# Optimization experiments

Measured on AMD Instinct MI355X. Metric: run time of the kernel, lower is better.

Reference implementation:

```python
import jax, jax.numpy as jnp
import numpy as np

L = 248      # max_clip_seq_len
WIN = 3      # window_size
H = 8        # attention heads
D = 768      # input/output dim
HID = 256    # rope hidden dim
SIGMA = 2.0
EPS_LN = 1e-5


def _layernorm(x, g, b):
    m = jnp.mean(x, axis=-1, keepdims=True)
    v = jnp.var(x, axis=-1, keepdims=True)
    return (x - m) / jnp.sqrt(v + EPS_LN) * g + b


def _normalize(x):
    n = jnp.linalg.norm(x, axis=-1, keepdims=True)
    return x / jnp.maximum(n, 1e-12)


def _peb_forward(word_feat, text_feat_full, word_pos, ctx_W, ctx_b, in_W, in_b,
                 out_W, out_b, cn_g, cn_b, r1_W, r1_b, ln_g, ln_b, r2_W, r2_b,
                 pos_emb, pos_temp):
    B, N, _ = word_feat.shape
    valid = word_pos != -1                              # [B,N] bool
    vf = valid.astype(word_feat.dtype)[..., None]       # [B,N,1]
    wp = jnp.clip(word_pos, 0, L - 1)                   # [B,N]
    half = WIN // 2
    offs = jnp.arange(-half, half + 1)
    positions = jnp.clip(wp[..., None] + offs[None, None, :], 0, L - 1)
    ctx = text_feat_full[jnp.arange(B)[:, None, None], positions]
    ctx_anchor = (ctx.reshape(B, N, WIN * D) @ ctx_W + ctx_b) * vf       # [B,N,D]
    q = word_feat * vf                                  # word_proj is Identity (768->768)
    # MultiheadAttention (batch_first), query=q, key=value=ctx_anchor
    hd = D // H
    qp = (q @ in_W[:, :D] + in_b[:D]).reshape(B, N, H, hd)
    kp = (ctx_anchor @ in_W[:, D:2 * D] + in_b[D:2 * D]).reshape(B, N, H, hd)
    vp = (ctx_anchor @ in_W[:, 2 * D:] + in_b[2 * D:]).reshape(B, N, H, hd)
    scores = jnp.einsum('bqhd,bkhd->bhqk', qp, kp) / jnp.sqrt(jnp.asarray(hd, q.dtype))
    attn = jax.nn.softmax(scores, axis=-1)
    ao = jnp.einsum('bhqk,bkhd->bqhd', attn, vp).reshape(B, N, D)
    attn_out = ao @ out_W + out_b
    x = _layernorm(q + attn_out, cn_g, cn_b) * vf       # word_feat_with_ctx
    # rope_mapping: Linear -> GELU -> LayerNorm -> Linear
    rope = _layernorm(jax.nn.gelu(x @ r1_W + r1_b, approximate=False), ln_g, ln_b) @ r2_W + r2_b
    rope_n = _normalize(rope)
    clip_ref_n = _normalize(pos_emb)                    # [L,D]
    temp = jnp.maximum(pos_temp, 0.001)
    logits = jnp.einsum('bnd,ld->bnl', rope_n, clip_ref_n) / temp
    log_q = jax.nn.log_softmax(logits, axis=-1)
    # gaussian soft target over L positions
    pos_idx = jnp.arange(L, dtype=jnp.float32)
    d2 = (pos_idx[None, None, :] - wp[..., None].astype(jnp.float32)) ** 2
    targ = jnp.exp(-d2 / (2.0 * SIGMA ** 2))
    targ = targ / (targ.sum(axis=-1, keepdims=True) + 1e-12)
    lqv = log_q * vf
    tv = targ * vf
    n_valid = valid.sum().astype(jnp.float32)
    safe_t = jnp.where(tv > 0, tv, 1.0)
    kl = jnp.sum(jnp.where(tv > 0, tv * (jnp.log(safe_t) - lqv), 0.0)) / (n_valid + 1e-12)
    # relative position loss on cosine similarity
    pos_sim01 = (jnp.einsum('bnd,bmd->bnm', rope_n, rope_n) + 1.0) / 2.0
    wpf = wp.astype(jnp.float32)
    target_sim = 1.0 - jnp.abs(wpf[:, :, None] - wpf[:, None, :]) / float(L)
    vm2 = vf[:, :, 0][:, None, :] * vf[:, :, 0][:, :, None]
    rel = jnp.sum((pos_sim01 * vm2 - target_sim * vm2) ** 2) / (vm2.sum() + 1e-12)
    peb_loss = (1.0 * kl + 0.5 * rel) * 1.0             # kl_weight=1, rel_weight=0.5, peb_weight=1
    # scatter blended positional features to 248-length sequence (vectorized over batch)
    vals = 0.8 * pos_emb[wp] + 0.2 * rope               # [B,N,D]
    pos_s = jnp.where(valid, wp, L)                     # invalid -> OOB index, dropped
    emb = jnp.zeros((B, L, D), word_feat.dtype).at[jnp.arange(B)[:, None], pos_s].set(vals, mode='drop')
    return emb, peb_loss, kl, rel


def setup_inputs() -> dict:
    key = jax.random.key(0)
    ks = jax.random.split(key, 20)
    B, N = 128, 128
    word_feat = jax.random.normal(ks[0], (B, N, D), jnp.float32)
    text_feat_full = jax.random.normal(ks[1], (B, L, D), jnp.float32)
    # unique sorted positions per batch (scatter is then deterministic, matching torch)
    perms = jax.vmap(lambda k: jax.random.permutation(k, L))(jax.random.split(ks[2], B))
    word_pos = jnp.sort(perms[:, :N], axis=-1).astype(jnp.int32)
    s = 0.02
    return {
        'word_feat': word_feat,
        'text_feat_full': text_feat_full,
        'word_pos': word_pos,
        'ctx_W': s * jax.random.normal(ks[3], (WIN * D, D), jnp.float32),
        'ctx_b': s * jax.random.normal(ks[4], (D,), jnp.float32),
        'in_W': s * jax.random.normal(ks[5], (D, 3 * D), jnp.float32),
        'in_b': s * jax.random.normal(ks[6], (3 * D,), jnp.float32),
        'out_W': s * jax.random.normal(ks[7], (D, D), jnp.float32),
        'out_b': s * jax.random.normal(ks[8], (D,), jnp.float32),
        'cn_g': jnp.ones((D,), jnp.float32) + s * jax.random.normal(ks[9], (D,), jnp.float32),
        'cn_b': s * jax.random.normal(ks[10], (D,), jnp.float32),
        'r1_W': s * jax.random.normal(ks[11], (D, HID), jnp.float32),
        'r1_b': s * jax.random.normal(ks[12], (HID,), jnp.float32),
        'ln_g': jnp.ones((HID,), jnp.float32) + s * jax.random.normal(ks[13], (HID,), jnp.float32),
        'ln_b': s * jax.random.normal(ks[14], (HID,), jnp.float32),
        'r2_W': s * jax.random.normal(ks[15], (HID, D), jnp.float32),
        'r2_b': s * jax.random.normal(ks[16], (D,), jnp.float32),
        'pos_emb': jax.random.normal(ks[17], (L, D), jnp.float32),
        'pos_temp': jnp.asarray(1.0, jnp.float32),
    }


def reference(word_feat, text_feat_full, word_pos, ctx_W, ctx_b, in_W, in_b,
              out_W, out_b, cn_g, cn_b, r1_W, r1_b, ln_g, ln_b, r2_W, r2_b,
              pos_emb, pos_temp):
    return _peb_forward(word_feat, text_feat_full, word_pos, ctx_W, ctx_b, in_W, in_b,
                        out_W, out_b, cn_g, cn_b, r1_W, r1_b, ln_g, ln_b, r2_W, r2_b,
                        pos_emb, pos_temp)
```

## Files before the change

### kernel.cpp

```cpp
#include <hip/hip_runtime.h>
#include <math.h>

#define BB   128
#define NN   128
#define LL   248
#define DD   768
#define HH   8
#define HDh  96
#define HIDN 256
#define MROWS (BB*NN)
#define MB_   (1u<<20)
#define KVLD 1536

typedef unsigned short u16;
typedef unsigned int   u32;
typedef __attribute__((ext_vector_type(8))) short s16x8;
typedef __attribute__((ext_vector_type(4))) float f32x4;

__device__ __forceinline__ u16 f2bf(float x) {
    u32 u = __float_as_uint(x);
    u32 r = u + 0x7fffu + ((u >> 16) & 1u);
    return (u16)(r >> 16);
}
__device__ __forceinline__ float bf2f(u16 h) {
    return __uint_as_float(((u32)h) << 16);
}
__device__ __forceinline__ void gload16(const void* g, void* l) {
    __builtin_amdgcn_global_load_lds(
        (const __attribute__((address_space(1))) void*)g,
        (__attribute__((address_space(3))) void*)l, 16, 0, 0);
}

template<int NT>
__device__ __forceinline__ float breduce_sum(float v, float* red) {
    const int tid = threadIdx.x;
    red[tid] = v; __syncthreads();
#pragma unroll
    for (int o = NT / 2; o > 0; o >>= 1) {
        if (tid < o) red[tid] += red[tid + o];
        __syncthreads();
    }
    float r = red[0]; __syncthreads();
    return r;
}
__device__ __forceinline__ double breduce_sum_d256(double v, double* red) {
    const int tid = threadIdx.x;
    red[tid] = v; __syncthreads();
#pragma unroll
    for (int o = 128; o > 0; o >>= 1) {
        if (tid < o) red[tid] += red[tid + o];
        __syncthreads();
    }
    double r = red[0]; __syncthreads();
    return r;
}

#define TEXT_N8 (BB*LL*DD/8)
#define Q_N8    (MROWS*(DD/8))
__global__ __launch_bounds__(256)
void prep_all_kernel(const float* __restrict__ ctx_W, u16* __restrict__ ctx_Wt,
                     const float* __restrict__ in_W,  u16* __restrict__ in_Wt,
                     const float* __restrict__ out_W, u16* __restrict__ out_Wt,
                     const float* __restrict__ r1_W,  u16* __restrict__ r1_Wt,
                     const float* __restrict__ r2_W,  u16* __restrict__ r2_Wt,
                     const float* __restrict__ text,  u16* __restrict__ textb,
                     const float* __restrict__ wf,    u16* __restrict__ qb,
                     const int* __restrict__ wpos,    int* __restrict__ cpos,
                     const float* __restrict__ pe,    u16* __restrict__ clipb) {
    __shared__ float smem[32 * 33];
    int bid = blockIdx.x;
    const int tid = threadIdx.x;

    if (bid < 4416) {
        const float* src; u16* dst; int C;
        if (bid < 1728)      { src = ctx_W; dst = ctx_Wt; C = 768;  }
        else if (bid < 3456) { src = in_W;  dst = in_Wt;  C = 2304; bid -= 1728; }
        else if (bid < 4032) { src = out_W; dst = out_Wt; C = 768;  bid -= 3456; }
        else if (bid < 4224) { src = r1_W;  dst = r1_Wt;  C = 256;  bid -= 4032; }
        else                 { src = r2_W;  dst = r2_Wt;  C = 768;  bid -= 4224; }
        const int R = (C == 768) ? ((dst == ctx_Wt) ? 2304 : ((dst == out_Wt) ? 768 : 256))
                                 : ((C == 2304) ? 768 : 768);
        const int ct = C >> 5;
        const int r0 = (bid / ct) * 32, c0 = (bid % ct) * 32;
        const int tx = tid & 31, ty = tid >> 5;
#pragma unroll
        for (int i = 0; i < 32; i += 8)
            smem[(ty + i) * 33 + tx] = src[(size_t)(r0 + ty + i) * C + c0 + tx];
        __syncthreads();
#pragma unroll
        for (int i = 0; i < 32; i += 8)
            dst[(size_t)(c0 + ty + i) * R + r0 + tx] = f2bf(smem[tx * 33 + ty + i]);
    } else if (bid < 4672) {
        const int l = bid - 4416;
        if (l >= LL) {
            for (int j = 0; j < 3; ++j) clipb[(size_t)l * DD + tid + j * 256] = 0;
            return;
        }
        float t[3]; float q = 0.f;
#pragma unroll
        for (int j = 0; j < 3; ++j) {
            t[j] = pe[(size_t)l * DD + tid + j * 256];
            q = fmaf(t[j], t[j], q);
        }
        q = breduce_sum<256>(q, smem);
        float inv = 1.f / fmaxf(sqrtf(q), 1e-12f);
#pragma unroll
        for (int j = 0; j < 3; ++j)
            clipb[(size_t)l * DD + tid + j * 256] = f2bf(t[j] * inv);
    } else {
        const int ebid = bid - 4672;
        if (ebid == 0) {
            for (int r = tid; r < MROWS; r += 256) {
                int w = wpos[r];
                cpos[r] = w < 0 ? 0 : (w > LL - 1 ? LL - 1 : w);
            }
        }
        const int TOT8 = TEXT_N8 + Q_N8;
        const int lane = tid & 63;
        const int wid = ebid * 4 + (tid >> 6);
        const int step = 2048 * 4 * 256;
        for (int base = wid * 256; base < TOT8; base += step) {
            if (base < TEXT_N8) {
                const float4* sp = (const float4*)text;
                float4 v[8]; int g[4];
#pragma unroll
                for (int j = 0; j < 4; ++j) {
                    g[j] = base + j * 64 + lane;
                    v[2*j]   = sp[2 * (size_t)g[j]];
                    v[2*j+1] = sp[2 * (size_t)g[j] + 1];
                }
#pragma unroll
                for (int j = 0; j < 4; ++j) {
                    uint4 o;
                    o.x = (u32)f2bf(v[2*j].x)   | ((u32)f2bf(v[2*j].y)   << 16);
                    o.y = (u32)f2bf(v[2*j].z)   | ((u32)f2bf(v[2*j].w)   << 16);
                    o.z = (u32)f2bf(v[2*j+1].x) | ((u32)f2bf(v[2*j+1].y) << 16);
                    o.w = (u32)f2bf(v[2*j+1].z) | ((u32)f2bf(v[2*j+1].w) << 16);
                    ((uint4*)textb)[g[j]] = o;
                }
            } else {
                const float4* sp = (const float4*)wf;
                float4 v[8]; int g[4]; float vfm[4];
#pragma unroll
                for (int j = 0; j < 4; ++j) {
                    g[j] = base + j * 64 + lane - TEXT_N8;
                    v[2*j]   = sp[2 * (size_t)g[j]];
                    v[2*j+1] = sp[2 * (size_t)g[j] + 1];
                }
#pragma unroll
                for (int j = 0; j < 4; ++j)
                    vfm[j] = (wpos[g[j] / 96] != -1) ? 1.f : 0.f;
#pragma unroll
                for (int j = 0; j < 4; ++j) {
                    uint4 o;
                    o.x = (u32)f2bf(v[2*j].x * vfm[j])   | ((u32)f2bf(v[2*j].y * vfm[j])   << 16);
                    o.y = (u32)f2bf(v[2*j].z * vfm[j])   | ((u32)f2bf(v[2*j].w * vfm[j])   << 16);
                    o.z = (u32)f2bf(v[2*j+1].x * vfm[j]) | ((u32)f2bf(v[2*j+1].y * vfm[j]) << 16);
                    o.w = (u32)f2bf(v[2*j+1].z * vfm[j]) | ((u32)f2bf(v[2*j+1].w * vfm[j]) << 16);
                    ((uint4*)qb)[g[j]] = o;
                }
            }
        }
    }
}

template<int GATHER, int CBF16, int MASK>
__global__ __launch_bounds__(256)
void gemm_bt(const u16* __restrict__ A,
             const u16* __restrict__ TXT,
             const int* __restrict__ cpos,
             const u16* __restrict__ Bt,
             const float* __restrict__ bias,
             void* __restrict__ Cout, int ldc, int K,
             const int* __restrict__ wpos) {
    __shared__ __align__(16) u16 Alds[128 * 64];
    __shared__ __align__(16) u16 Blds[128 * 64];
    const int tid = threadIdx.x;
    const int l = tid & 63, wv = tid >> 6;

    const int gx  = gridDim.x;
    const int hw  = blockIdx.y * gx + blockIdx.x;
    const int nwg = gx * gridDim.y;
    const int cpx = nwg >> 3;
    const int lin = (hw & 7) * cpx + (hw >> 3);
    const int m0 = (lin / gx) * 128, n0 = (lin % gx) * 128;

    const int rw = wv * 8 + (l >> 3);
    const int ce = ((l & 7) ^ (l >> 3)) << 3;
    u16* Ad0 = Alds + wv * 512;
    u16* Bd0 = Blds + wv * 512;

    const int wm = (wv >> 1) * 64, wn = (wv & 1) * 64;
    const int la = l & 15, lg = l >> 4;

    int aoff[4], boff[4];
#pragma unroll
    for (int m = 0; m < 4; ++m) {
        int ra = wm + m * 16 + la;
        aoff[m] = ra * 64 + (((lg ^ (la & 7)) << 3));
        int rb = wn + m * 16 + la;
        boff[m] = rb * 64 + (((lg ^ (la & 7)) << 3));
    }

    const u16* pb[4];
#pragma unroll
    for (int i = 0; i < 4; ++i)
        pb[i] = Bt + (size_t)(n0 + rw + i * 32) * K + ce;

    f32x4 acc[4][4] = {};

    auto do_step = [&](const u16* a0, const u16* a1, const u16* a2, const u16* a3,
                       const u16* b0, const u16* b1, const u16* b2, const u16* b3) {
        gload16(a0, Ad0);
        gload16(a1, Ad0 + 2048);
        gload16(a2, Ad0 + 4096);
        gload16(a3, Ad0 + 6144);
        gload16(b0, Bd0);
        gload16(b1, Bd0 + 2048);
        gload16(b2, Bd0 + 4096);
        gload16(b3, Bd0 + 6144);
        __syncthreads();
#pragma unroll
        for (int kk = 0; kk < 2; ++kk) {
            const int kx = kk << 5;
            s16x8 af[4], bf[4];
#pragma unroll
            for (int m = 0; m < 4; ++m) af[m] = *(const s16x8*)(Alds + (aoff[m] ^ kx));
#pragma unroll
            for (int n = 0; n < 4; ++n) bf[n] = *(const s16x8*)(Blds + (boff[n] ^ kx));
#pragma unroll
            for (int m = 0; m < 4; ++m)
#pragma unroll
                for (int n = 0; n < 4; ++n)
                    acc[m][n] = __builtin_amdgcn_mfma_f32_16x16x32_bf16(
                        af[m], bf[n], acc[m][n], 0, 0, 0);
        }
        __syncthreads();
    };

    if constexpr (GATHER) {
        int gb[4], gc[4];
#pragma unroll
        for (int i = 0; i < 4; ++i) {
            int g = m0 + rw + i * 32;
            gb[i] = g >> 7;
            gc[i] = cpos[g];
        }
#pragma unroll 1
        for (int w = 0; w < 3; ++w) {
            const u16* pa[4];
#pragma unroll
            for (int i = 0; i < 4; ++i) {
                int p = gc[i] + w - 1;
                p = p < 0 ? 0 : (p > LL - 1 ? LL - 1 : p);
                pa[i] = TXT + ((size_t)(gb[i] * LL + p)) * DD + ce;
            }
            const u16* b0 = pb[0] + w * DD; const u16* b1 = pb[1] + w * DD;
            const u16* b2 = pb[2] + w * DD; const u16* b3 = pb[3] + w * DD;
#pragma unroll 1
            for (int kt = 0; kt < 12; ++kt)
                do_step(pa[0] + kt * 64, pa[1] + kt * 64, pa[2] + kt * 64, pa[3] + kt * 64,
                        b0 + kt * 64, b1 + kt * 64, b2 + kt * 64, b3 + kt * 64);
        }
    } else {
        const u16* pa[4];
#pragma unroll
        for (int i = 0; i < 4; ++i)
            pa[i] = A + (size_t)(m0 + rw + i * 32) * K + ce;
        const int nk = K >> 6;
#pragma unroll 1
        for (int kt = 0; kt < nk; ++kt)
            do_step(pa[0] + kt * 64, pa[1] + kt * 64, pa[2] + kt * 64, pa[3] + kt * 64,
                    pb[0] + kt * 64, pb[1] + kt * 64, pb[2] + kt * 64, pb[3] + kt * 64);
    }

#pragma unroll
    for (int m = 0; m < 4; ++m) {
        const int rb = m0 + wm + m * 16 + lg * 4;
        float vf[4];
        if constexpr (MASK) {
#pragma unroll
            for (int r = 0; r < 4; ++r) vf[r] = (wpos[rb + r] != -1) ? 1.f : 0.f;
        }
#pragma unroll
        for (int n = 0; n < 4; ++n) {
            const int col = n0 + wn + n * 16 + la;
            const float bv = bias[col];
#pragma unroll
            for (int r = 0; r < 4; ++r) {
                float o = acc[m][n][r] + bv;
                if constexpr (MASK) o *= vf[r];
                if constexpr (CBF16)
                    ((u16*)Cout)[(size_t)(rb + r) * ldc + col] = f2bf(o);
                else
                    ((float*)Cout)[(size_t)(rb + r) * ldc + col] = o;
            }
        }
    }
}

__global__ __launch_bounds__(512)
void attn_mfma_kernel(const u16* __restrict__ qp, const u16* __restrict__ kvb,
                      u16* __restrict__ ao) {
    __shared__ __align__(16) u16 K_lds[128 * 96];
    __shared__ __align__(16) u16 Vt_lds[96 * 128];
    __shared__ __align__(16) u16 P_lds[128 * 128];
    const int bh = blockIdx.x;
    const int b = bh >> 3, h = bh & 7;
    const int tid = threadIdx.x;
    const int l = tid & 63, wv = tid >> 6;
    const int la = l & 15, lg = l >> 4;
    const float scale = 0.10206207261596575f;

    const size_t qbase  = ((size_t)b * NN) * DD + h * HDh;
    const size_t kvbase = ((size_t)b * NN) * KVLD + h * HDh;

#pragma unroll
    for (int i = 0; i < 3; ++i) {
        int f = i * 8192 + wv * 1024 + l * 16;
        int row = f / 192;
        int inner = f - row * 192;
        gload16((const char*)(kvb + kvbase + (size_t)row * KVLD) + inner,
                (char*)K_lds + f);
    }

    uint4 vchunk[3]; int vkey[3], vd0[3];
#pragma unroll
    for (int i = 0; i < 3; ++i) {
        int c = tid + i * 512;
        int key = c / 12, dc = c - key * 12;
        vkey[i] = key; vd0[i] = dc * 8;
        vchunk[i] = *(const uint4*)(kvb + kvbase + (size_t)key * KVLD + DD + dc * 8);
    }

    const int q0 = wv * 16;
    s16x8 qf[3];
#pragma unroll
    for (int kt = 0; kt < 3; ++kt)
        qf[kt] = *(const s16x8*)(qp + qbase + (size_t)(q0 + la) * DD + kt * 32 + lg * 8);

#pragma unroll
    for (int i = 0; i < 3; ++i) {
        const u16* e = (const u16*)&vchunk[i];
#pragma unroll
        for (int j = 0; j < 8; ++j) {
            int d = vd0[i] + j;
            int byte = ((d * 128 + vkey[i]) * 2) ^ ((d & 7) << 4);
            *(u16*)((char*)Vt_lds + byte) = e[j];
        }
    }
    __syncthreads();

    f32x4 sacc[8] = {};
#pragma unroll
    for (int kt = 0; kt < 3; ++kt) {
#pragma unroll
        for (int nf = 0; nf < 8; ++nf) {
            s16x8 bfr = *(const s16x8*)(K_lds + (nf * 16 + la) * 96 + kt * 32 + lg * 8);
            sacc[nf] = __builtin_amdgcn_mfma_f32_16x16x32_bf16(qf[kt], bfr, sacc[nf], 0, 0, 0);
        }
    }

#pragma unroll
    for (int r = 0; r < 4; ++r) {
        float m = -1e30f;
#pragma unroll
        for (int nf = 0; nf < 8; ++nf) m = fmaxf(m, sacc[nf][r]);
#pragma unroll
        for (int o = 8; o > 0; o >>= 1) m = fmaxf(m, __shfl_xor(m, o, 64));
        m *= scale;
        float p[8]; float s = 0.f;
#pragma unroll
        for (int nf = 0; nf < 8; ++nf) { p[nf] = expf(sacc[nf][r] * scale - m); s += p[nf]; }
#pragma unroll
        for (int o = 8; o > 0; o >>= 1) s += __shfl_xor(s, o, 64);
        const float inv = 1.f / s;
        const int q = q0 + lg * 4 + r;
#pragma unroll
        for (int nf = 0; nf < 8; ++nf) {
            int byte = ((q * 128 + nf * 16 + la) * 2) ^ ((q & 7) << 4);
            *(u16*)((char*)P_lds + byte) = f2bf(p[nf] * inv);
        }
    }
    __syncthreads();

    f32x4 oacc[6] = {};
#pragma unroll
    for (int kk = 0; kk < 4; ++kk) {
        const int qrow = q0 + la;
        int abyte = ((qrow * 128 + kk * 32 + lg * 8) * 2) ^ ((qrow & 7) << 4);
        s16x8 af = *(const s16x8*)((char*)P_lds + abyte);
#pragma unroll
        for (int nf = 0; nf < 6; ++nf) {
            const int d = nf * 16 + la;
            int bbyte = ((d * 128 + kk * 32 + lg * 8) * 2) ^ ((d & 7) << 4);
            s16x8 bfr = *(const s16x8*)((char*)Vt_lds + bbyte);
            oacc[nf] = __builtin_amdgcn_mfma_f32_16x16x32_bf16(af, bfr, oacc[nf], 0, 0, 0);
        }
    }

#pragma unroll
    for (int nf = 0; nf < 6; ++nf) {
#pragma unroll
        for (int r = 0; r < 4; ++r) {
            const int q = q0 + lg * 4 + r;
            ao[qbase + (size_t)q * DD + nf * 16 + la] = f2bf(oacc[nf][r]);
        }
    }
}

__global__ __launch_bounds__(256)
void ln768_kernel(const u16* __restrict__ qb, const u16* __restrict__ at,
                  const int* __restrict__ wpos, const float* __restrict__ g,
                  const float* __restrict__ bta, u16* __restrict__ xout) {
    __shared__ float red[256];
    const int r = blockIdx.x, tid = threadIdx.x;
    const float vf = (wpos[r] != -1) ? 1.f : 0.f;
    float t[3]; float s = 0.f, q = 0.f;
#pragma unroll
    for (int j = 0; j < 3; ++j) {
        int d = tid + j * 256;
        t[j] = bf2f(qb[(size_t)r * DD + d]) + bf2f(at[(size_t)r * DD + d]);
        s += t[j];
        q = fmaf(t[j], t[j], q);
    }
    s = breduce_sum<256>(s, red);
    q = breduce_sum<256>(q, red);
    float mean = s * (1.f / DD);
    float var  = q * (1.f / DD) - mean * mean;
    float inv  = 1.f / sqrtf(var + 1e-5f);
#pragma unroll
    for (int j = 0; j < 3; ++j) {
        int d = tid + j * 256;
        xout[(size_t)r * DD + d] = f2bf(((t[j] - mean) * inv * g[d] + bta[d]) * vf);
    }
}

__global__ __launch_bounds__(256)
void ln256_gelu_kernel(const u16* __restrict__ g1, const float* __restrict__ lg,
                       const float* __restrict__ lb, u16* __restrict__ hout) {
    __shared__ float red[256];
    const int r = blockIdx.x, tid = threadIdx.x;
    float v  = bf2f(g1[(size_t)r * HIDN + tid]);
    float ge = 0.5f * v * (1.f + erff(v * 0.7071067811865475f));
    float s = breduce_sum<256>(ge, red);
    float q = breduce_sum<256>(ge * ge, red);
    float mean = s * (1.f / HIDN);
    float var  = q * (1.f / HIDN) - mean * mean;
    float inv  = 1.f / sqrtf(var + 1e-5f);
    hout[(size_t)r * HIDN + tid] = f2bf((ge - mean) * inv * lg[tid] + lb[tid]);
}

__global__ __launch_bounds__(256)
void norm_scatter_kernel(const u16* __restrict__ ropeb, const float* __restrict__ pe,
                         const int* __restrict__ wpos, u16* __restrict__ rnb,
                         float* __restrict__ emb) {
    __shared__ float red[256];
    const int r = blockIdx.x, tid = threadIdx.x;
    float t[3]; float q = 0.f;
#pragma unroll
    for (int j = 0; j < 3; ++j) {
        t[j] = bf2f(ropeb[(size_t)r * DD + tid + j * 256]);
        q = fmaf(t[j], t[j], q);
    }
    q = breduce_sum<256>(q, red);
    float inv = 1.f / fmaxf(sqrtf(q), 1e-12f);
    const int wr = wpos[r];
    const bool valid = (wr != -1);
    const int wp = wr < 0 ? 0 : (wr > LL - 1 ? LL - 1 : wr);
    const int b = r >> 7;
#pragma unroll
    for (int j = 0; j < 3; ++j) {
        int d = tid + j * 256;
        rnb[(size_t)r * DD + d] = f2bf(t[j] * inv);
        if (valid)
            emb[((size_t)b * LL + wp) * DD + d] =
                0.8f * pe[(size_t)wp * DD + d] + 0.2f * t[j];
    }
}

__global__ __launch_bounds__(256)
void kl_lite_kernel(const float* __restrict__ logits, const int* __restrict__ wpos,
                    const float* __restrict__ pos_temp, float* __restrict__ klp) {
    const int row = blockIdx.x * 4 + (threadIdx.x >> 6);
    const int l = threadIdx.x & 63;
    const float invt = 1.f / fmaxf(pos_temp[0], 0.001f);
    const float* lrow = logits + (size_t)row * 256;

    float lg[4];
#pragma unroll
    for (int q = 0; q < 4; ++q) {
        int c = l + q * 64;
        lg[q] = (c < LL) ? lrow[c] * invt : -1e30f;
    }
    float m = fmaxf(fmaxf(lg[0], lg[1]), fmaxf(lg[2], lg[3]));
#pragma unroll
    for (int o = 32; o > 0; o >>= 1) m = fmaxf(m, __shfl_xor(m, o, 64));

    float S = 0.f;
#pragma unroll
    for (int q = 0; q < 4; ++q) S += expf(lg[q] - m);
#pragma unroll
    for (int o = 32; o > 0; o >>= 1) S += __shfl_xor(S, o, 64);
    const float logZ = m + logf(S);

    const int wr = wpos[row];
    const bool valid = (wr != -1);
    const int wp = wr < 0 ? 0 : (wr > LL - 1 ? LL - 1 : wr);

    float targ[4]; float tsum = 0.f;
#pragma unroll
    for (int q = 0; q < 4; ++q) {
        int c = l + q * 64;
        float dl = (float)c - (float)wp;
        targ[q] = (c < LL) ? expf(-dl * dl * 0.125f) : 0.f;
        tsum += targ[q];
    }
#pragma unroll
    for (int o = 32; o > 0; o >>= 1) tsum += __shfl_xor(tsum, o, 64);
    const float tden = 1.f / (tsum + 1e-12f);

    float c_ = 0.f;
#pragma unroll
    for (int q = 0; q < 4; ++q) {
        float tn = targ[q] * tden;
        if (valid && tn > 0.f) c_ += tn * (logf(tn) - (lg[q] - logZ));
    }
#pragma unroll
    for (int o = 32; o > 0; o >>= 1) c_ += __shfl_xor(c_, o, 64);
    if (l == 0) klp[row] = c_;
}

__global__ __launch_bounds__(512)
void rel_mfma_kernel(const u16* __restrict__ rnb, const int* __restrict__ wpos,
                     float* __restrict__ rel_part, float* __restrict__ vm2_part) {
    __shared__ __align__(16) u16 T[128 * 32];
    __shared__ float red[512];
    const int blk = blockIdx.x;
    const int b = blk >> 1, jh = blk & 1;
    const int tid = threadIdx.x;
    const int l = tid & 63, wv = tid >> 6;
    const int la = l & 15, lg = l >> 4;

    const int f = wv * 1024 + l * 16;
    const int rA = f >> 6;
    const int cb = (f & 63) ^ (((rA >> 1) & 3) << 4);
    const int ce = cb >> 1;
    const u16* src = rnb + ((size_t)(b * NN + rA)) * DD + ce;
    u16* dst = T + wv * 512;

    const int ra = wv * 16 + la;
    const int aoff = ra * 32 + ((lg * 8) ^ (((ra >> 1) & 3) << 3));
    int boff[4];
#pragma unroll
    for (int nf = 0; nf < 4; ++nf) {
        int rb = jh * 64 + nf * 16 + la;
        boff[nf] = rb * 32 + ((lg * 8) ^ (((rb >> 1) & 3) << 3));
    }

    f32x4 acc[4] = {};
    for (int kt = 0; kt < 24; ++kt) {
        gload16(src + kt * 32, dst);
        __syncthreads();
        s16x8 a = *(const s16x8*)(T + aoff);
        s16x8 bf_[4];
#pragma unroll
        for (int nf = 0; nf < 4; ++nf) bf_[nf] = *(const s16x8*)(T + boff[nf]);
#pragma unroll
        for (int nf = 0; nf < 4; ++nf)
            acc[nf] = __builtin_amdgcn_mfma_f32_16x16x32_bf16(a, bf_[nf], acc[nf], 0, 0, 0);
        __syncthreads();
    }

    float wif[4], vi[4];
#pragma unroll
    for (int r = 0; r < 4; ++r) {
        int wi = wpos[b * NN + wv * 16 + lg * 4 + r];
        vi[r] = (wi != -1) ? 1.f : 0.f;
        wif[r] = (float)(wi < 0 ? 0 : (wi > LL - 1 ? LL - 1 : wi));
    }
    float csum = 0.f, msum = 0.f;
#pragma unroll
    for (int nf = 0; nf < 4; ++nf) {
        int wj = wpos[b * NN + jh * 64 + nf * 16 + la];
        float vj = (wj != -1) ? 1.f : 0.f;
        float wjf = (float)(wj < 0 ? 0 : (wj > LL - 1 ? LL - 1 : wj));
#pragma unroll
        for (int r = 0; r < 4; ++r) {
            float sim = (acc[nf][r] + 1.f) * 0.5f;
            float ts  = 1.f - fabsf(wif[r] - wjf) * (1.f / (float)LL);
            float m2  = vi[r] * vj;
            float df  = m2 * (sim - ts);
            csum += df * df;
            msum += m2;
        }
    }
    csum = breduce_sum<512>(csum, red);
    msum = breduce_sum<512>(msum, red);
    if (tid == 0) { rel_part[blk] = csum; vm2_part[blk] = msum; }
}

__global__ __launch_bounds__(256)
void final_kernel(const float* __restrict__ klp, const float* __restrict__ relp,
                  const float* __restrict__ vmp, const int* __restrict__ wpos,
                  float* __restrict__ outs) {
    __shared__ double rd[256];
    const int tid = threadIdx.x;
    double kl = 0.0, rel = 0.0, vm = 0.0, nv = 0.0;
    for (int r = tid; r < MROWS; r += 256) {
        kl += (double)klp[r];
        nv += (wpos[r] != -1) ? 1.0 : 0.0;
    }
    if (tid < 256) {
        rel += (double)relp[tid];
        vm  += (double)vmp[tid];
    }
    kl  = breduce_sum_d256(kl, rd);
    rel = breduce_sum_d256(rel, rd);
    vm  = breduce_sum_d256(vm, rd);
    nv  = breduce_sum_d256(nv, rd);
    if (tid == 0) {
        float klf  = (float)(kl / (nv + 1e-12));
        float relf = (float)(rel / (vm + 1e-12));
        outs[0] = klf + 0.5f * relf;
        outs[1] = klf;
        outs[2] = relf;
    }
}

extern "C" void kernel_launch(void* const* d_in, const int* in_sizes, int n_in,
                              void* d_out, int out_size, void* d_ws, size_t ws_size,
                              hipStream_t stream) {
    (void)in_sizes; (void)n_in; (void)ws_size;

    const float* word_feat = (const float*)d_in[0];
    const float* text      = (const float*)d_in[1];
    const int*   wpos      = (const int*)d_in[2];
    const float* ctx_W     = (const float*)d_in[3];
    const float* ctx_b     = (const float*)d_in[4];
    const float* in_W      = (const float*)d_in[5];
    const float* in_b      = (const float*)d_in[6];
    const float* out_W     = (const float*)d_in[7];
    const float* out_b     = (const float*)d_in[8];
    const float* cn_g      = (const float*)d_in[9];
    const float* cn_b      = (const float*)d_in[10];
    const float* r1_W      = (const float*)d_in[11];
    const float* r1_b      = (const float*)d_in[12];
    const float* ln_g      = (const float*)d_in[13];
    const float* ln_b      = (const float*)d_in[14];
    const float* r2_W      = (const float*)d_in[15];
    const float* r2_b      = (const float*)d_in[16];
    const float* pos_emb   = (const float*)d_in[17];
    const float* pos_temp  = (const float*)d_in[18];

    char* W = (char*)d_ws;
    u16*   ctx_Wt = (u16*)(W);
    u16*   in_Wt  = ctx_Wt + (size_t)768 * 2304;
    u16*   out_Wt = in_Wt  + (size_t)2304 * 768;
    u16*   r1_Wt  = out_Wt + (size_t)768 * 768;
    u16*   r2_Wt  = r1_Wt  + (size_t)256 * 768;
    u16*   clipb  = r2_Wt + (size_t)768 * 256;
    int*   cposb  = (int*)(clipb + (size_t)256 * DD);
    float* klp    = (float*)(cposb + MROWS);
    float* relp   = klp + MROWS;
    float* vmp    = relp + 256;
    float* zbias  = vmp + 256;
    u16*   textb  = (u16*)(W + (size_t)12 * MB_);
    u16*   atoutb = textb;
    float* logits = (float*)(W + (size_t)12 * MB_);
    u16*   xb     = (u16*)(W + (size_t)36 * MB_);
    u16*   qb     = (u16*)(W + (size_t)60 * MB_);
    u16*   ctxa   = (u16*)(W + (size_t)86 * MB_);
    u16*   aob    = ctxa;
    u16*   rnb    = ctxa;
    u16*   qpb    = (u16*)(W + (size_t)112 * MB_);
    u16*   g1b    = (u16*)(W + (size_t)112 * MB_);
    u16*   hb     = (u16*)(W + (size_t)128 * MB_);
    u16*   kvb    = (u16*)(W + (size_t)138 * MB_);
    u16*   ropeb  = kvb;

    hipMemsetAsync(d_out, 0, (size_t)out_size * sizeof(float), stream);
    hipMemsetAsync(zbias, 0, 256 * sizeof(float), stream);

    dim3 blk(256);

    prep_all_kernel<<<dim3(4416 + 256 + 2048), blk, 0, stream>>>(
        ctx_W, ctx_Wt, in_W, in_Wt, out_W, out_Wt, r1_W, r1_Wt, r2_W, r2_Wt,
        text, textb, word_feat, qb, wpos, cposb, pos_emb, clipb);

    dim3 g768(6, 128);
    dim3 g1536(12, 128);
    dim3 g256(2, 128);

    gemm_bt<1, 1, 1><<<g768, blk, 0, stream>>>(
        nullptr, textb, cposb, ctx_Wt, ctx_b, ctxa, DD, 3 * DD, wpos);
    gemm_bt<0, 1, 0><<<g768, blk, 0, stream>>>(
        qb, nullptr, nullptr, in_Wt, in_b, qpb, DD, DD, nullptr);
    gemm_bt<0, 1, 0><<<g1536, blk, 0, stream>>>(
        ctxa, nullptr, nullptr, in_Wt + (size_t)768 * 768, in_b + DD, kvb, KVLD, DD, nullptr);
    attn_mfma_kernel<<<dim3(BB * HH), dim3(512), 0, stream>>>(qpb, kvb, aob);
    gemm_bt<0, 1, 0><<<g768, blk, 0, stream>>>(
        aob, nullptr, nullptr, out_Wt, out_b, atoutb, DD, DD, nullptr);
    ln768_kernel<<<dim3(MROWS), blk, 0, stream>>>(qb, atoutb, wpos, cn_g, cn_b, xb);
    gemm_bt<0, 1, 0><<<g256, blk, 0, stream>>>(
        xb, nullptr, nullptr, r1_Wt, r1_b, g1b, HIDN, DD, nullptr);
    ln256_gelu_kernel<<<dim3(MROWS), blk, 0, stream>>>(g1b, ln_g, ln_b, hb);
    gemm_bt<0, 1, 0><<<g768, blk, 0, stream>>>(
        hb, nullptr, nullptr, r2_Wt, r2_b, ropeb, DD, HIDN, nullptr);
    norm_scatter_kernel<<<dim3(MROWS), blk, 0, stream>>>(
        ropeb, pos_emb, wpos, rnb, (float*)d_out);
    gemm_bt<0, 0, 0><<<g256, blk, 0, stream>>>(
        rnb, nullptr, nullptr, clipb, zbias, logits, 256, DD, nullptr);
    kl_lite_kernel<<<dim3(MROWS / 4), blk, 0, stream>>>(logits, wpos, pos_temp, klp);
    rel_mfma_kernel<<<dim3(BB * 2), dim3(512), 0, stream>>>(rnb, wpos, relp, vmp);
    final_kernel<<<dim3(1), blk, 0, stream>>>(
        klp, relp, vmp, wpos, (float*)d_out + (size_t)BB * LL * DD);
}
```

Measured before the change: 453.0 us.

## Fuse text fp32-to-bf16 conversion into gathered context GEMM A-tile loads

The separate pass that converts the whole text feature tensor to bf16 in the prep kernel is removed. The gather GEMM now reads fp32 text rows directly through registers, converts them with packed bf16 intrinsics, and writes them into a swizzled LDS layout. The aim is to drop a large round trip through global memory (about 24 MB written and later reread) and shrink the prep grid. The cost is that the gather GEMM's A loads become synchronous register loads at twice the byte width, and each text row is reread up to three times for the window. Packed bf16 conversion intrinsics also replace the manual rounding in the word-feature conversion.

Measured after the change: 468.7 us. +3.5%, slower.

```diff
diff --git a/kernel.cpp b/kernel.cpp
--- a/kernel.cpp
+++ b/kernel.cpp
@@ -1,4 +1,5 @@
 #include <hip/hip_runtime.h>
+#include <hip/hip_bf16.h>
 #include <math.h>
 
 #define BB   128
@@ -25,6 +26,11 @@
 __device__ __forceinline__ float bf2f(u16 h) {
     return __uint_as_float(((u32)h) << 16);
 }
+__device__ __forceinline__ u32 pk2bf(float a, float b) {
+    __hip_bfloat162 h = __float22bfloat162_rn(make_float2(a, b));
+    u32 r; __builtin_memcpy(&r, &h, 4);
+    return r;
+}
 __device__ __forceinline__ void gload16(const void* g, void* l) {
     __builtin_amdgcn_global_load_lds(
         (const __attribute__((address_space(1))) void*)g,
@@ -55,7 +61,6 @@
     return r;
 }
 
-#define TEXT_N8 (BB*LL*DD/8)
 #define Q_N8    (MROWS*(DD/8))
 __global__ __launch_bounds__(256)
 void prep_all_kernel(const float* __restrict__ ctx_W, u16* __restrict__ ctx_Wt,
@@ -63,7 +68,6 @@
                      const float* __restrict__ out_W, u16* __restrict__ out_Wt,
                      const float* __restrict__ r1_W,  u16* __restrict__ r1_Wt,
                      const float* __restrict__ r2_W,  u16* __restrict__ r2_Wt,
-                     const float* __restrict__ text,  u16* __restrict__ textb,
                      const float* __restrict__ wf,    u16* __restrict__ qb,
                      const int* __restrict__ wpos,    int* __restrict__ cpos,
                      const float* __restrict__ pe,    u16* __restrict__ clipb) {
@@ -79,7 +83,7 @@
         else if (bid < 4224) { src = r1_W;  dst = r1_Wt;  C = 256;  bid -= 4032; }
         else                 { src = r2_W;  dst = r2_Wt;  C = 768;  bid -= 4224; }
         const int R = (C == 768) ? ((dst == ctx_Wt) ? 2304 : ((dst == out_Wt) ? 768 : 256))
-                                 : ((C == 2304) ? 768 : 768);
+                                 : 768;
         const int ct = C >> 5;
         const int r0 = (bid / ct) * 32, c0 = (bid % ct) * 32;
         const int tx = tid & 31, ty = tid >> 5;
@@ -115,50 +119,29 @@
                 cpos[r] = w < 0 ? 0 : (w > LL - 1 ? LL - 1 : w);
             }
         }
-        const int TOT8 = TEXT_N8 + Q_N8;
         const int lane = tid & 63;
         const int wid = ebid * 4 + (tid >> 6);
-        const int step = 2048 * 4 * 256;
-        for (int base = wid * 256; base < TOT8; base += step) {
-            if (base < TEXT_N8) {
-                const float4* sp = (const float4*)text;
-                float4 v[8]; int g[4];
-#pragma unroll
-                for (int j = 0; j < 4; ++j) {
-                    g[j] = base + j * 64 + lane;
-                    v[2*j]   = sp[2 * (size_t)g[j]];
-                    v[2*j+1] = sp[2 * (size_t)g[j] + 1];
-                }
-#pragma unroll
-                for (int j = 0; j < 4; ++j) {
-                    uint4 o;
-                    o.x = (u32)f2bf(v[2*j].x)   | ((u32)f2bf(v[2*j].y)   << 16);
-                    o.y = (u32)f2bf(v[2*j].z)   | ((u32)f2bf(v[2*j].w)   << 16);
-                    o.z = (u32)f2bf(v[2*j+1].x) | ((u32)f2bf(v[2*j+1].y) << 16);
-                    o.w = (u32)f2bf(v[2*j+1].z) | ((u32)f2bf(v[2*j+1].w) << 16);
-                    ((uint4*)textb)[g[j]] = o;
-                }
-            } else {
-                const float4* sp = (const float4*)wf;
-                float4 v[8]; int g[4]; float vfm[4];
-#pragma unroll
-                for (int j = 0; j < 4; ++j) {
-                    g[j] = base + j * 64 + lane - TEXT_N8;
-                    v[2*j]   = sp[2 * (size_t)g[j]];
-                    v[2*j+1] = sp[2 * (size_t)g[j] + 1];
-                }
-#pragma unroll
-                for (int j = 0; j < 4; ++j)
-                    vfm[j] = (wpos[g[j] / 96] != -1) ? 1.f : 0.f;
-#pragma unroll
-                for (int j = 0; j < 4; ++j) {
-                    uint4 o;
-                    o.x = (u32)f2bf(v[2*j].x * vfm[j])   | ((u32)f2bf(v[2*j].y * vfm[j])   << 16);
-                    o.y = (u32)f2bf(v[2*j].z * vfm[j])   | ((u32)f2bf(v[2*j].w * vfm[j])   << 16);
-                    o.z = (u32)f2bf(v[2*j+1].x * vfm[j]) | ((u32)f2bf(v[2*j+1].y * vfm[j]) << 16);
-                    o.w = (u32)f2bf(v[2*j+1].z * vfm[j]) | ((u32)f2bf(v[2*j+1].w * vfm[j]) << 16);
-                    ((uint4*)qb)[g[j]] = o;
-                }
+        const int step = 1024 * 4 * 256;
+        for (int base = wid * 256; base < Q_N8; base += step) {
+            const float4* sp = (const float4*)wf;
+            float4 v[8]; int g[4]; float vfm[4];
+#pragma unroll
+            for (int j = 0; j < 4; ++j) {
+                g[j] = base + j * 64 + lane;
+                v[2*j]   = sp[2 * (size_t)g[j]];
+                v[2*j+1] = sp[2 * (size_t)g[j] + 1];
+            }
+#pragma unroll
+            for (int j = 0; j < 4; ++j)
+                vfm[j] = (wpos[g[j] / 96] != -1) ? 1.f : 0.f;
+#pragma unroll
+            for (int j = 0; j < 4; ++j) {
+                uint4 o;
+                o.x = pk2bf(v[2*j].x * vfm[j],   v[2*j].y * vfm[j]);
+                o.y = pk2bf(v[2*j].z * vfm[j],   v[2*j].w * vfm[j]);
+                o.z = pk2bf(v[2*j+1].x * vfm[j], v[2*j+1].y * vfm[j]);
+                o.w = pk2bf(v[2*j+1].z * vfm[j], v[2*j+1].w * vfm[j]);
+                ((uint4*)qb)[g[j]] = o;
             }
         }
     }
@@ -167,7 +150,7 @@
 template<int GATHER, int CBF16, int MASK>
 __global__ __launch_bounds__(256)
 void gemm_bt(const u16* __restrict__ A,
-             const u16* __restrict__ TXT,
+             const float* __restrict__ TXT,
              const int* __restrict__ cpos,
              const u16* __restrict__ Bt,
              const float* __restrict__ bias,
@@ -209,17 +192,7 @@
 
     f32x4 acc[4][4] = {};
 
-    auto do_step = [&](const u16* a0, const u16* a1, const u16* a2, const u16* a3,
-                       const u16* b0, const u16* b1, const u16* b2, const u16* b3) {
-        gload16(a0, Ad0);
-        gload16(a1, Ad0 + 2048);
-        gload16(a2, Ad0 + 4096);
-        gload16(a3, Ad0 + 6144);
-        gload16(b0, Bd0);
-        gload16(b1, Bd0 + 2048);
-        gload16(b2, Bd0 + 4096);
-        gload16(b3, Bd0 + 6144);
-        __syncthreads();
+    auto mfma_body = [&]() {
 #pragma unroll
         for (int kk = 0; kk < 2; ++kk) {
             const int kx = kk << 5;
@@ -235,32 +208,54 @@
                     acc[m][n] = __builtin_amdgcn_mfma_f32_16x16x32_bf16(
                         af[m], bf[n], acc[m][n], 0, 0, 0);
         }
-        __syncthreads();
     };
 
     if constexpr (GATHER) {
+        const int s  = l & 7;
+        const int rl = l >> 3;
+        u16* awr = Alds + (wv * 8 + rl) * 64 + ((s ^ rl) << 3);
         int gb[4], gc[4];
 #pragma unroll
         for (int i = 0; i < 4; ++i) {
-            int g = m0 + rw + i * 32;
-            gb[i] = g >> 7;
-            gc[i] = cpos[g];
+            int g = m0 + i * 32 + wv * 8 + rl;
+            gb[i] = g >> 7; gc[i] = cpos[g];
         }
 #pragma unroll 1
         for (int w = 0; w < 3; ++w) {
-            const u16* pa[4];
+            const float* pa[4];
 #pragma unroll
             for (int i = 0; i < 4; ++i) {
-                int p = gc[i] + w - 1;
-                p = p < 0 ? 0 : (p > LL - 1 ? LL - 1 : p);
-                pa[i] = TXT + ((size_t)(gb[i] * LL + p)) * DD + ce;
+                int p = gc[i] + w - 1; p = p < 0 ? 0 : (p > LL - 1 ? LL - 1 : p);
+                pa[i] = TXT + ((size_t)(gb[i] * LL + p)) * DD + s * 8;
             }
             const u16* b0 = pb[0] + w * DD; const u16* b1 = pb[1] + w * DD;
             const u16* b2 = pb[2] + w * DD; const u16* b3 = pb[3] + w * DD;
 #pragma unroll 1
-            for (int kt = 0; kt < 12; ++kt)
-                do_step(pa[0] + kt * 64, pa[1] + kt * 64, pa[2] + kt * 64, pa[3] + kt * 64,
-                        b0 + kt * 64, b1 + kt * 64, b2 + kt * 64, b3 + kt * 64);
+            for (int kt = 0; kt < 12; ++kt) {
+                const int k0 = kt * 64;
+                gload16(b0 + k0, Bd0);
+                gload16(b1 + k0, Bd0 + 2048);
+                gload16(b2 + k0, Bd0 + 4096);
+                gload16(b3 + k0, Bd0 + 6144);
+                float4 v0[4], v1[4];
+#pragma unroll
+                for (int i = 0; i < 4; ++i) {
+                    v0[i] = *(const float4*)(pa[i] + k0);
+                    v1[i] = *(const float4*)(pa[i] + k0 + 4);
+                }
+#pragma unroll
+                for (int i = 0; i < 4; ++i) {
+                    uint4 o;
+                    o.x = pk2bf(v0[i].x, v0[i].y);
+                    o.y = pk2bf(v0[i].z, v0[i].w);
+                    o.z = pk2bf(v1[i].x, v1[i].y);
+                    o.w = pk2bf(v1[i].z, v1[i].w);
+                    *(uint4*)(awr + i * 2048) = o;
+                }
+                __syncthreads();
+                mfma_body();
+                __syncthreads();
+            }
         }
     } else {
         const u16* pa[4];
@@ -269,9 +264,20 @@
             pa[i] = A + (size_t)(m0 + rw + i * 32) * K + ce;
         const int nk = K >> 6;
 #pragma unroll 1
-        for (int kt = 0; kt < nk; ++kt)
-            do_step(pa[0] + kt * 64, pa[1] + kt * 64, pa[2] + kt * 64, pa[3] + kt * 64,
-                    pb[0] + kt * 64, pb[1] + kt * 64, pb[2] + kt * 64, pb[3] + kt * 64);
+        for (int kt = 0; kt < nk; ++kt) {
+            const int k0 = kt << 6;
+            gload16(pa[0] + k0, Ad0);
+            gload16(pa[1] + k0, Ad0 + 2048);
+            gload16(pa[2] + k0, Ad0 + 4096);
+            gload16(pa[3] + k0, Ad0 + 6144);
+            gload16(pb[0] + k0, Bd0);
+            gload16(pb[1] + k0, Bd0 + 2048);
+            gload16(pb[2] + k0, Bd0 + 4096);
+            gload16(pb[3] + k0, Bd0 + 6144);
+            __syncthreads();
+            mfma_body();
+            __syncthreads();
+        }
     }
 
 #pragma unroll
@@ -665,8 +671,7 @@
     float* relp   = klp + MROWS;
     float* vmp    = relp + 256;
     float* zbias  = vmp + 256;
-    u16*   textb  = (u16*)(W + (size_t)12 * MB_);
-    u16*   atoutb = textb;
+    u16*   atoutb = (u16*)(W + (size_t)12 * MB_);
     float* logits = (float*)(W + (size_t)12 * MB_);
     u16*   xb     = (u16*)(W + (size_t)36 * MB_);
     u16*   qb     = (u16*)(W + (size_t)60 * MB_);
@@ -684,16 +689,16 @@
 
     dim3 blk(256);
 
-    prep_all_kernel<<<dim3(4416 + 256 + 2048), blk, 0, stream>>>(
+    prep_all_kernel<<<dim3(4416 + 256 + 1024), blk, 0, stream>>>(
         ctx_W, ctx_Wt, in_W, in_Wt, out_W, out_Wt, r1_W, r1_Wt, r2_W, r2_Wt,
-        text, textb, word_feat, qb, wpos, cposb, pos_emb, clipb);
+        word_feat, qb, wpos, cposb, pos_emb, clipb);
 
     dim3 g768(6, 128);
     dim3 g1536(12, 128);
     dim3 g256(2, 128);
 
     gemm_bt<1, 1, 1><<<g768, blk, 0, stream>>>(
-        nullptr, textb, cposb, ctx_Wt, ctx_b, ctxa, DD, 3 * DD, wpos);
+        nullptr, text, cposb, ctx_Wt, ctx_b, ctxa, DD, 3 * DD, wpos);
     gemm_bt<0, 1, 0><<<g768, blk, 0, stream>>>(
         qb, nullptr, nullptr, in_Wt, in_b, qpb, DD, DD, nullptr);
     gemm_bt<0, 1, 0><<<g1536, blk, 0, stream>>>(
```
